# Kernel optimization log

Hardware: AMD Instinct MI355X
Metric: run time of the kernel (lower is better)

## Reference

```python
import jax, jax.numpy as jnp
import numpy as np
import math

D_MODEL = 512
N_HEADS = 8
D_K = D_MODEL // N_HEADS
B, S = 2, 4096
LN_EPS = 1e-5


def _xavier(key, fan_in, fan_out):
    limit = math.sqrt(6.0 / (fan_in + fan_out))
    return jax.random.uniform(key, (fan_in, fan_out), jnp.float32, -limit, limit)


def setup_inputs() -> dict:
    key = jax.random.key(0)
    ks = jax.random.split(key, 12)
    x = jax.random.normal(ks[0], (B, S, D_MODEL), jnp.float32)
    consciousness_state = jax.random.normal(ks[1], (B, D_MODEL), jnp.float32)
    # weights stored as [in, out] (equivalent to torch Linear weight.T)
    w_q = _xavier(ks[2], D_MODEL, D_MODEL)
    w_k = _xavier(ks[3], D_MODEL, D_MODEL)
    w_v = _xavier(ks[4], D_MODEL, D_MODEL)
    w_o = _xavier(ks[5], D_MODEL, D_MODEL)
    b_o = jnp.zeros((D_MODEL,), jnp.float32)
    w_gate = _xavier(ks[6], D_MODEL, N_HEADS)
    b_gate = jnp.zeros((N_HEADS,), jnp.float32)
    w_int = _xavier(ks[7], D_MODEL, D_MODEL)
    b_int = jnp.zeros((D_MODEL,), jnp.float32)
    ln_gamma = jnp.ones((D_MODEL,), jnp.float32)
    ln_beta = jnp.zeros((D_MODEL,), jnp.float32)
    return {"x": x, "consciousness_state": consciousness_state,
            "w_q": w_q, "w_k": w_k, "w_v": w_v, "w_o": w_o, "b_o": b_o,
            "w_gate": w_gate, "b_gate": b_gate, "w_int": w_int, "b_int": b_int,
            "ln_gamma": ln_gamma, "ln_beta": ln_beta}


def reference(x, consciousness_state, w_q, w_k, w_v, w_o, b_o,
              w_gate, b_gate, w_int, b_int, ln_gamma, ln_beta):
    b, s, d = x.shape
    # project and split heads: [B, H, S, d_k]
    def heads(w):
        return (x @ w).reshape(b, s, N_HEADS, D_K).transpose(0, 2, 1, 3)
    Q, K, V = heads(w_q), heads(w_k), heads(w_v)
    scores = jnp.einsum('bhsd,bhtd->bhst', Q, K) / math.sqrt(D_K)  # [B,H,S,S]
    # per-head consciousness gate BEFORE softmax
    cw = jax.nn.sigmoid(consciousness_state @ w_gate + b_gate)  # [B,H]
    scores = scores * cw[:, :, None, None]
    attn = jax.nn.softmax(scores, axis=-1)
    # dropout is identity in eval mode
    context = jnp.einsum('bhst,bhtd->bhsd', attn, V)
    context = context.transpose(0, 2, 1, 3).reshape(b, s, d)
    out = context @ w_o + b_o
    iw = jax.nn.sigmoid(consciousness_state @ w_int + b_int)  # [B,D]
    out = out * iw[:, None, :]
    # residual + LayerNorm
    h = out + x
    mu = jnp.mean(h, axis=-1, keepdims=True)
    var = jnp.var(h, axis=-1, keepdims=True)
    out = (h - mu) * jax.lax.rsqrt(var + LN_EPS) * ln_gamma + ln_beta
    return out, attn.mean(axis=1)
```

## Files before the change

### kernel.cpp

```cpp
#include <hip/hip_runtime.h>
#include <hip/hip_bf16.h>

using short8 = __attribute__((ext_vector_type(8))) short;
using f32x4  = __attribute__((ext_vector_type(4))) float;

#define S_LEN 4096
#define DM 512

__device__ __forceinline__ unsigned short f2b(float f) {
    unsigned int u = __float_as_uint(f);
    u += 0x7fffu + ((u >> 16) & 1u);
    return (unsigned short)(u >> 16);
}

__device__ __forceinline__ short8 pack8(float4 a, float4 b) {
    short8 r;
    r[0] = (short)f2b(a.x); r[1] = (short)f2b(a.y); r[2] = (short)f2b(a.z); r[3] = (short)f2b(a.w);
    r[4] = (short)f2b(b.x); r[5] = (short)f2b(b.y); r[6] = (short)f2b(b.z); r[7] = (short)f2b(b.w);
    return r;
}

__global__ __launch_bounds__(256) void convert_w(
    const float* __restrict__ w0, const float* __restrict__ w1,
    const float* __restrict__ w2, const float* __restrict__ w3,
    unsigned short* __restrict__ t0, unsigned short* __restrict__ t1,
    unsigned short* __restrict__ t2, unsigned short* __restrict__ t3)
{
    __shared__ float sh[64][65];
    const float* src; unsigned short* dst;
    switch (blockIdx.z) {
        case 0: src = w0; dst = t0; break;
        case 1: src = w1; dst = t1; break;
        case 2: src = w2; dst = t2; break;
        default: src = w3; dst = t3; break;
    }
    int k0 = blockIdx.x * 64, n0 = blockIdx.y * 64;
    int tid = threadIdx.x;
    for (int i = tid; i < 4096; i += 256) {
        int k = i >> 6, n = i & 63;
        sh[k][n] = src[(size_t)(k0 + k) * DM + n0 + n];
    }
    __syncthreads();
    for (int i = tid; i < 4096; i += 256) {
        int n = i >> 6, k = i & 63;
        dst[(size_t)(n0 + n) * DM + k0 + k] = f2b(sh[k][n]);
    }
}

__global__ __launch_bounds__(256) void convert_x(
    const float* __restrict__ x, unsigned short* __restrict__ xb)
{
    size_t i = ((size_t)blockIdx.x * 256 + threadIdx.x) * 8;
    float4 a = *reinterpret_cast<const float4*>(x + i);
    float4 b = *reinterpret_cast<const float4*>(x + i + 4);
    *reinterpret_cast<short8*>(xb + i) = pack8(a, b);
}

__global__ __launch_bounds__(64) void gates_kernel(
    const float* __restrict__ cs, const float* __restrict__ wg, const float* __restrict__ bg,
    const float* __restrict__ wi, const float* __restrict__ bi,
    float* __restrict__ cwout, float* __restrict__ iwout)
{
    int o = blockIdx.x, b = blockIdx.y, lane = threadIdx.x;
    const float* c = cs + (size_t)b * DM;
    float acc = 0.f;
    if (o < 8) {
        #pragma unroll
        for (int j = 0; j < 8; ++j) { int k = j * 64 + lane; acc += c[k] * wg[(size_t)k * 8 + o]; }
    } else {
        int n = o - 8;
        #pragma unroll
        for (int j = 0; j < 8; ++j) { int k = j * 64 + lane; acc += c[k] * wi[(size_t)k * DM + n]; }
    }
    #pragma unroll
    for (int d = 32; d; d >>= 1) acc += __shfl_xor(acc, d);
    if (lane == 0) {
        if (o < 8) cwout[b * 8 + o] = 1.f / (1.f + __expf(-(acc + bg[o])));
        else       iwout[b * DM + (o - 8)] = 1.f / (1.f + __expf(-(acc + bi[o - 8])));
    }
}

__global__ __launch_bounds__(256) void gemm_qkv(
    const unsigned short* __restrict__ A, const unsigned short* __restrict__ WT,
    const float* __restrict__ cw,
    unsigned short* __restrict__ Qb, unsigned short* __restrict__ Kb,
    unsigned short* __restrict__ Vt)
{
    __shared__ unsigned short a_sh[64][72];
    __shared__ unsigned short b_sh[64][72];
    const int m0 = blockIdx.x * 64;
    const int n0g = blockIdx.y * 64;
    const int which = blockIdx.y >> 3;
    const int tid = threadIdx.x;
    const int wave = tid >> 6, lane = tid & 63;
    const int g = lane >> 4, lr = lane & 15;
    const int srow = tid >> 3, skc = (tid & 7) * 8;

    float sq = 1.f;
    if (which == 0) {
        int b = blockIdx.x >> 6;
        int h = blockIdx.y & 7;
        sq = cw[b * 8 + h] * 0.125f * 1.44269504f;
    }

    f32x4 acc[4];
    #pragma unroll
    for (int i = 0; i < 4; ++i) acc[i] = (f32x4){0.f, 0.f, 0.f, 0.f};

    short8 ar[2], br[2];
    #pragma unroll
    for (int cc = 0; cc < 2; ++cc) {
        int row = srow + cc * 32;
        ar[cc] = *reinterpret_cast<const short8*>(A  + (size_t)(m0  + row) * DM + skc);
        br[cc] = *reinterpret_cast<const short8*>(WT + (size_t)(n0g + row) * DM + skc);
    }

    for (int k0 = 0; k0 < 512; k0 += 64) {
        #pragma unroll
        for (int cc = 0; cc < 2; ++cc) {
            int row = srow + cc * 32;
            *reinterpret_cast<short8*>(&a_sh[row][skc]) = ar[cc];
            *reinterpret_cast<short8*>(&b_sh[row][skc]) = br[cc];
        }
        __syncthreads();
        if (k0 + 64 < 512) {
            #pragma unroll
            for (int cc = 0; cc < 2; ++cc) {
                int row = srow + cc * 32;
                ar[cc] = *reinterpret_cast<const short8*>(A  + (size_t)(m0  + row) * DM + k0 + 64 + skc);
                br[cc] = *reinterpret_cast<const short8*>(WT + (size_t)(n0g + row) * DM + k0 + 64 + skc);
            }
        }
        __builtin_amdgcn_s_setprio(1);
        #pragma unroll
        for (int ks = 0; ks < 2; ++ks) {
            short8 af = *reinterpret_cast<const short8*>(&a_sh[wave * 16 + lr][ks * 32 + g * 8]);
            #pragma unroll
            for (int nf = 0; nf < 4; ++nf) {
                short8 bf = *reinterpret_cast<const short8*>(&b_sh[nf * 16 + lr][ks * 32 + g * 8]);
                acc[nf] = __builtin_amdgcn_mfma_f32_16x16x32_bf16(af, bf, acc[nf], 0, 0, 0);
            }
        }
        __builtin_amdgcn_s_setprio(0);
        __syncthreads();
    }

    #pragma unroll
    for (int nf = 0; nf < 4; ++nf) {
        #pragma unroll
        for (int r = 0; r < 4; ++r) {
            int m = m0 + wave * 16 + g * 4 + r;
            int nl = (blockIdx.y & 7) * 64 + nf * 16 + lr;
            unsigned short v = f2b(acc[nf][r] * sq);
            if (which == 0) {
                Qb[(size_t)m * DM + nl] = v;
            } else if (which == 1) {
                Kb[(size_t)m * DM + nl] = v;
            } else {
                int b = m >> 12, s = m & 4095;
                int h = nl >> 6, d = nl & 63;
                Vt[((size_t)(b * 8 + h) * 64 + d) * S_LEN + s] = v;
            }
        }
    }
}

__global__ __launch_bounds__(256) void gemm_proj(
    const unsigned short* __restrict__ A, const unsigned short* __restrict__ WT,
    float* __restrict__ outf, const float* __restrict__ bias,
    const float* __restrict__ iw, const float* __restrict__ xres)
{
    __shared__ unsigned short a_sh[64][72];
    __shared__ unsigned short b_sh[64][72];
    const int m0 = blockIdx.x * 64;
    const int n0 = blockIdx.y * 64;
    const int tid = threadIdx.x;
    const int wave = tid >> 6, lane = tid & 63;
    const int g = lane >> 4, lr = lane & 15;
    const int srow = tid >> 3, skc = (tid & 7) * 8;

    f32x4 acc[4];
    #pragma unroll
    for (int i = 0; i < 4; ++i) acc[i] = (f32x4){0.f, 0.f, 0.f, 0.f};

    short8 ar[2], br[2];
    #pragma unroll
    for (int cc = 0; cc < 2; ++cc) {
        int row = srow + cc * 32;
        ar[cc] = *reinterpret_cast<const short8*>(A  + (size_t)(m0 + row) * DM + skc);
        br[cc] = *reinterpret_cast<const short8*>(WT + (size_t)(n0 + row) * DM + skc);
    }

    for (int k0 = 0; k0 < 512; k0 += 64) {
        #pragma unroll
        for (int cc = 0; cc < 2; ++cc) {
            int row = srow + cc * 32;
            *reinterpret_cast<short8*>(&a_sh[row][skc]) = ar[cc];
            *reinterpret_cast<short8*>(&b_sh[row][skc]) = br[cc];
        }
        __syncthreads();
        if (k0 + 64 < 512) {
            #pragma unroll
            for (int cc = 0; cc < 2; ++cc) {
                int row = srow + cc * 32;
                ar[cc] = *reinterpret_cast<const short8*>(A  + (size_t)(m0 + row) * DM + k0 + 64 + skc);
                br[cc] = *reinterpret_cast<const short8*>(WT + (size_t)(n0 + row) * DM + k0 + 64 + skc);
            }
        }
        __builtin_amdgcn_s_setprio(1);
        #pragma unroll
        for (int ks = 0; ks < 2; ++ks) {
            short8 af = *reinterpret_cast<const short8*>(&a_sh[wave * 16 + lr][ks * 32 + g * 8]);
            #pragma unroll
            for (int nf = 0; nf < 4; ++nf) {
                short8 bf = *reinterpret_cast<const short8*>(&b_sh[nf * 16 + lr][ks * 32 + g * 8]);
                acc[nf] = __builtin_amdgcn_mfma_f32_16x16x32_bf16(af, bf, acc[nf], 0, 0, 0);
            }
        }
        __builtin_amdgcn_s_setprio(0);
        __syncthreads();
    }

    #pragma unroll
    for (int nf = 0; nf < 4; ++nf) {
        #pragma unroll
        for (int r = 0; r < 4; ++r) {
            int m = m0 + wave * 16 + g * 4 + r;
            int n = n0 + nf * 16 + lr;
            int b = m >> 12;
            float v = (acc[nf][r] + bias[n]) * iw[b * DM + n] + xres[(size_t)m * DM + n];
            outf[(size_t)m * DM + n] = v;
        }
    }
}

__global__ __launch_bounds__(256) void attn_ctx(
    const unsigned short* __restrict__ Qb, const unsigned short* __restrict__ Kb,
    const unsigned short* __restrict__ Vt,
    float* __restrict__ lbuf, unsigned short* __restrict__ ctx)
{
    __shared__ unsigned short k_sh[64][72];
    __shared__ unsigned short v_sh[64][72];
    __shared__ unsigned short p_sh[4][32][72];
    const int wg = blockIdx.x;
    const int logical = (wg & 7) * 64 + (wg >> 3);
    const int q0 = (logical & 31) * 128;
    const int bh = logical >> 5;
    const int b = bh >> 3, h = bh & 7;
    const int tid = threadIdx.x, wave = tid >> 6, lane = tid & 63;
    const int g = lane >> 4, lr = lane & 15;
    const int srow = tid >> 3, skc = (tid & 7) * 8;

    short8 qf[2][2];
    #pragma unroll
    for (int qq = 0; qq < 2; ++qq) {
        const unsigned short* qp = Qb + (size_t)(b * S_LEN + q0 + wave * 32 + qq * 16 + lr) * DM + h * 64;
        qf[qq][0] = *reinterpret_cast<const short8*>(qp + g * 8);
        qf[qq][1] = *reinterpret_cast<const short8*>(qp + 32 + g * 8);
    }
    short8 onesb;
    #pragma unroll
    for (int i = 0; i < 8; ++i) onesb[i] = (short)0x3F80;

    f32x4 lsum[2];
    f32x4 cacc[2][4];
    #pragma unroll
    for (int qq = 0; qq < 2; ++qq) {
        lsum[qq] = (f32x4){0.f, 0.f, 0.f, 0.f};
        #pragma unroll
        for (int i = 0; i < 4; ++i) cacc[qq][i] = (f32x4){0.f, 0.f, 0.f, 0.f};
    }

    const unsigned short* Kbase = Kb + (size_t)(b * S_LEN) * DM + h * 64;
    const unsigned short* Vbase = Vt + ((size_t)bh * 64) * S_LEN;

    short8 kr[2], vr[2];
    #pragma unroll
    for (int cc = 0; cc < 2; ++cc) {
        int row = srow + cc * 32;
        kr[cc] = *reinterpret_cast<const short8*>(Kbase + (size_t)row * DM + skc);
        vr[cc] = *reinterpret_cast<const short8*>(Vbase + (size_t)row * S_LEN + skc);
    }

    for (int kv0 = 0; kv0 < S_LEN; kv0 += 64) {
        #pragma unroll
        for (int cc = 0; cc < 2; ++cc) {
            int row = srow + cc * 32;
            *reinterpret_cast<short8*>(&k_sh[row][skc]) = kr[cc];
            *reinterpret_cast<short8*>(&v_sh[row][skc]) = vr[cc];
        }
        __syncthreads();
        f32x4 st[2][4];
        #pragma unroll
        for (int qq = 0; qq < 2; ++qq)
            #pragma unroll
            for (int f = 0; f < 4; ++f) st[qq][f] = (f32x4){0.f, 0.f, 0.f, 0.f};
        __builtin_amdgcn_s_setprio(1);
        #pragma unroll
        for (int ks = 0; ks < 2; ++ks) {
            #pragma unroll
            for (int f = 0; f < 4; ++f) {
                short8 kf = *reinterpret_cast<const short8*>(&k_sh[f * 16 + lr][ks * 32 + g * 8]);
                #pragma unroll
                for (int qq = 0; qq < 2; ++qq)
                    st[qq][f] = __builtin_amdgcn_mfma_f32_16x16x32_bf16(kf, qf[qq][ks], st[qq][f], 0, 0, 0);
            }
        }
        __builtin_amdgcn_s_setprio(0);
        if (kv0 + 64 < S_LEN) {
            #pragma unroll
            for (int cc = 0; cc < 2; ++cc) {
                int row = srow + cc * 32;
                kr[cc] = *reinterpret_cast<const short8*>(Kbase + (size_t)(kv0 + 64 + row) * DM + skc);
                vr[cc] = *reinterpret_cast<const short8*>(Vbase + (size_t)row * S_LEN + kv0 + 64 + skc);
            }
        }
        #pragma unroll
        for (int qq = 0; qq < 2; ++qq) {
            #pragma unroll
            for (int f = 0; f < 4; ++f) {
                float p0 = __builtin_amdgcn_exp2f(st[qq][f][0]);
                float p1 = __builtin_amdgcn_exp2f(st[qq][f][1]);
                float p2 = __builtin_amdgcn_exp2f(st[qq][f][2]);
                float p3 = __builtin_amdgcn_exp2f(st[qq][f][3]);
                unsigned u0, u1;
                asm("v_cvt_pk_bf16_f32 %0, %1, %2" : "=v"(u0) : "v"(p0), "v"(p1));
                asm("v_cvt_pk_bf16_f32 %0, %1, %2" : "=v"(u1) : "v"(p2), "v"(p3));
                uint2 pv; pv.x = u0; pv.y = u1;
                *reinterpret_cast<uint2*>(&p_sh[wave][qq * 16 + lr][f * 16 + g * 4]) = pv;
            }
        }
        __builtin_amdgcn_s_setprio(1);
        #pragma unroll
        for (int ks = 0; ks < 2; ++ks) {
            short8 pf[2];
            #pragma unroll
            for (int qq = 0; qq < 2; ++qq)
                pf[qq] = *reinterpret_cast<const short8*>(&p_sh[wave][qq * 16 + lr][ks * 32 + g * 8]);
            #pragma unroll
            for (int qq = 0; qq < 2; ++qq)
                lsum[qq] = __builtin_amdgcn_mfma_f32_16x16x32_bf16(pf[qq], onesb, lsum[qq], 0, 0, 0);
            #pragma unroll
            for (int df = 0; df < 4; ++df) {
                short8 vf = *reinterpret_cast<const short8*>(&v_sh[df * 16 + lr][ks * 32 + g * 8]);
                #pragma unroll
                for (int qq = 0; qq < 2; ++qq)
                    cacc[qq][df] = __builtin_amdgcn_mfma_f32_16x16x32_bf16(pf[qq], vf, cacc[qq][df], 0, 0, 0);
            }
        }
        __builtin_amdgcn_s_setprio(0);
        __syncthreads();
    }
    #pragma unroll
    for (int qq = 0; qq < 2; ++qq) {
        float rl[4];
        #pragma unroll
        for (int r = 0; r < 4; ++r) rl[r] = 1.f / lsum[qq][r];
        if (lr == 0) {
            #pragma unroll
            for (int r = 0; r < 4; ++r)
                lbuf[bh * S_LEN + q0 + wave * 32 + qq * 16 + g * 4 + r] = lsum[qq][r];
        }
        #pragma unroll
        for (int df = 0; df < 4; ++df) {
            #pragma unroll
            for (int r = 0; r < 4; ++r) {
                int q = q0 + wave * 32 + qq * 16 + g * 4 + r;
                ctx[(size_t)(b * S_LEN + q) * DM + h * 64 + df * 16 + lr] = f2b(cacc[qq][df][r] * rl[r]);
            }
        }
    }
}

__global__ __launch_bounds__(256) void attn_mean(
    const unsigned short* __restrict__ Qb, const unsigned short* __restrict__ Kb,
    const float* __restrict__ lbuf, float* __restrict__ outmean)
{
    __shared__ unsigned short k_sh[32][520];
    const int wg = blockIdx.x;
    const int logical = (wg & 7) * 128 + (wg >> 3);
    const int q0 = (logical & 63) * 64;
    const int kcb = logical >> 6;
    const int kc0 = (kcb & 7) * 512;
    const int b = kcb >> 3;
    const int tid = threadIdx.x, wave = tid >> 6, lane = tid & 63;
    const int g = lane >> 4, lr = lane & 15;
    const int srow = tid >> 6, scol = (tid & 63) * 8;

    const int qrow = q0 + wave * 16 + lr;
    float la2[8];
    #pragma unroll
    for (int h = 0; h < 8; ++h)
        la2[h] = -log2f(lbuf[(b * 8 + h) * S_LEN + qrow]) - 3.0f;

    const unsigned short* qbase = Qb + (size_t)(b * S_LEN + qrow) * DM;
    const unsigned short* Kbase = Kb + (size_t)(b * S_LEN) * DM;
    float* obase = outmean + (size_t)(b * S_LEN + qrow) * S_LEN;

    short8 stg[8];
    #pragma unroll
    for (int i = 0; i < 8; ++i) {
        int row = srow + i * 4;
        stg[i] = *reinterpret_cast<const short8*>(Kbase + (size_t)(kc0 + row) * DM + scol);
    }

    for (int t = 0; t < 16; ++t) {
        int kv0 = kc0 + t * 32;
        #pragma unroll
        for (int i = 0; i < 8; ++i) {
            int row = srow + i * 4;
            *reinterpret_cast<short8*>(&k_sh[row][scol]) = stg[i];
        }
        __syncthreads();
        if (t + 1 < 16) {
            #pragma unroll
            for (int i = 0; i < 8; ++i) {
                int row = srow + i * 4;
                stg[i] = *reinterpret_cast<const short8*>(Kbase + (size_t)(kv0 + 32 + row) * DM + scol);
            }
        }
        float macc[2][4];
        #pragma unroll
        for (int f = 0; f < 2; ++f)
            #pragma unroll
            for (int r = 0; r < 4; ++r) macc[f][r] = 0.f;
        #pragma unroll
        for (int h = 0; h < 8; ++h) {
            const unsigned short* qp = qbase + h * 64;
            short8 qf0 = *reinterpret_cast<const short8*>(qp + g * 8);
            short8 qf1 = *reinterpret_cast<const short8*>(qp + 32 + g * 8);
            f32x4 s[2];
            s[0] = (f32x4){0.f, 0.f, 0.f, 0.f};
            s[1] = (f32x4){0.f, 0.f, 0.f, 0.f};
            __builtin_amdgcn_s_setprio(1);
            #pragma unroll
            for (int f = 0; f < 2; ++f) {
                short8 kf0 = *reinterpret_cast<const short8*>(&k_sh[f * 16 + lr][h * 64 + g * 8]);
                s[f] = __builtin_amdgcn_mfma_f32_16x16x32_bf16(kf0, qf0, s[f], 0, 0, 0);
                short8 kf1 = *reinterpret_cast<const short8*>(&k_sh[f * 16 + lr][h * 64 + 32 + g * 8]);
                s[f] = __builtin_amdgcn_mfma_f32_16x16x32_bf16(kf1, qf1, s[f], 0, 0, 0);
            }
            __builtin_amdgcn_s_setprio(0);
            #pragma unroll
            for (int f = 0; f < 2; ++f)
                #pragma unroll
                for (int r = 0; r < 4; ++r)
                    macc[f][r] += __builtin_amdgcn_exp2f(s[f][r] + la2[h]);
        }
        #pragma unroll
        for (int f = 0; f < 2; ++f) {
            float4 ov;
            ov.x = macc[f][0]; ov.y = macc[f][1]; ov.z = macc[f][2]; ov.w = macc[f][3];
            *reinterpret_cast<float4*>(obase + kv0 + f * 16 + g * 4) = ov;
        }
        __syncthreads();
    }
}

__global__ __launch_bounds__(64) void ln_kernel(
    const float* __restrict__ hbuf, const float* __restrict__ gamma,
    const float* __restrict__ beta, float* __restrict__ dout)
{
    int row = blockIdx.x, lane = threadIdx.x;
    const float* hp = hbuf + (size_t)row * DM + lane * 8;
    float4 v0 = *reinterpret_cast<const float4*>(hp);
    float4 v1 = *reinterpret_cast<const float4*>(hp + 4);
    float s = v0.x + v0.y + v0.z + v0.w + v1.x + v1.y + v1.z + v1.w;
    float ss = v0.x * v0.x + v0.y * v0.y + v0.z * v0.z + v0.w * v0.w
             + v1.x * v1.x + v1.y * v1.y + v1.z * v1.z + v1.w * v1.w;
    #pragma unroll
    for (int d = 32; d; d >>= 1) { s += __shfl_xor(s, d); ss += __shfl_xor(ss, d); }
    float mu = s * (1.f / 512.f);
    float var = ss * (1.f / 512.f) - mu * mu;
    float rstd = rsqrtf(var + 1e-5f);
    float4 g0 = *reinterpret_cast<const float4*>(gamma + lane * 8);
    float4 g1 = *reinterpret_cast<const float4*>(gamma + lane * 8 + 4);
    float4 b0 = *reinterpret_cast<const float4*>(beta + lane * 8);
    float4 b1 = *reinterpret_cast<const float4*>(beta + lane * 8 + 4);
    float4 o0, o1;
    o0.x = (v0.x - mu) * rstd * g0.x + b0.x;
    o0.y = (v0.y - mu) * rstd * g0.y + b0.y;
    o0.z = (v0.z - mu) * rstd * g0.z + b0.z;
    o0.w = (v0.w - mu) * rstd * g0.w + b0.w;
    o1.x = (v1.x - mu) * rstd * g1.x + b1.x;
    o1.y = (v1.y - mu) * rstd * g1.y + b1.y;
    o1.z = (v1.z - mu) * rstd * g1.z + b1.z;
    o1.w = (v1.w - mu) * rstd * g1.w + b1.w;
    float* op = dout + (size_t)row * DM + lane * 8;
    *reinterpret_cast<float4*>(op) = o0;
    *reinterpret_cast<float4*>(op + 4) = o1;
}

extern "C" void kernel_launch(void* const* d_in, const int* in_sizes, int n_in,
                              void* d_out, int out_size, void* d_ws, size_t ws_size,
                              hipStream_t stream)
{
    const float* x   = (const float*)d_in[0];
    const float* cs  = (const float*)d_in[1];
    const float* wq  = (const float*)d_in[2];
    const float* wk  = (const float*)d_in[3];
    const float* wv  = (const float*)d_in[4];
    const float* wo  = (const float*)d_in[5];
    const float* bo  = (const float*)d_in[6];
    const float* wg  = (const float*)d_in[7];
    const float* bg  = (const float*)d_in[8];
    const float* wi  = (const float*)d_in[9];
    const float* bi  = (const float*)d_in[10];
    const float* gam = (const float*)d_in[11];
    const float* bet = (const float*)d_in[12];

    float* out = (float*)d_out;
    float* outmean = out + (size_t)2 * S_LEN * DM;

    char* ws = (char*)d_ws;
    size_t off = 0;
    auto alloc = [&](size_t bytes) { void* p = ws + off; off += (bytes + 255) & ~(size_t)255; return p; };

    unsigned short* wtq = (unsigned short*)alloc((size_t)DM * DM * 2);
    unsigned short* wtk = (unsigned short*)alloc((size_t)DM * DM * 2);
    unsigned short* wtv = (unsigned short*)alloc((size_t)DM * DM * 2);
    unsigned short* wto = (unsigned short*)alloc((size_t)DM * DM * 2);
    unsigned short* xb  = (unsigned short*)alloc((size_t)2 * S_LEN * DM * 2);
    unsigned short* Qb  = (unsigned short*)alloc((size_t)2 * S_LEN * DM * 2);
    unsigned short* Kb  = (unsigned short*)alloc((size_t)2 * S_LEN * DM * 2);
    unsigned short* Vt  = (unsigned short*)alloc((size_t)2 * S_LEN * DM * 2);
    unsigned short* ctx = (unsigned short*)alloc((size_t)2 * S_LEN * DM * 2);
    float* lbuf = (float*)alloc((size_t)16 * S_LEN * 4);
    float* cwb  = (float*)alloc(64);
    float* iwb  = (float*)alloc((size_t)2 * DM * 4);
    float* hbuf = (float*)Qb;

    convert_w<<<dim3(8, 8, 4), 256, 0, stream>>>(wq, wk, wv, wo, wtq, wtk, wtv, wto);
    convert_x<<<dim3(2048), 256, 0, stream>>>(x, xb);
    gates_kernel<<<dim3(520, 2), 64, 0, stream>>>(cs, wg, bg, wi, bi, cwb, iwb);

    gemm_qkv<<<dim3(128, 24), 256, 0, stream>>>(xb, wtq, cwb, Qb, Kb, Vt);

    attn_ctx<<<dim3(512), 256, 0, stream>>>(Qb, Kb, Vt, lbuf, ctx);
    attn_mean<<<dim3(1024), 256, 0, stream>>>(Qb, Kb, lbuf, outmean);

    gemm_proj<<<dim3(128, 8), 256, 0, stream>>>(ctx, wto, hbuf, bo, iwb, x);
    ln_kernel<<<dim3(2 * S_LEN), 64, 0, stream>>>(hbuf, gam, bet, out);
}
```

Baseline: 243.6 us.

## Double-buffer K/V shared tiles in attention context kernel to drop a barrier

Turns the K/V shared-memory tiles into two ping-pong buffers. Each iteration now writes the prefetched next tile into the spare buffer after the PV MFMAs, and global loads run two tiles ahead. This removes one __syncthreads per iteration and gives the global loads more time before they are needed. In exchange it doubles K/V LDS use, which may lower occupancy, and keeps the prefetch registers live longer.

Result: no change. 245.4 us (+0.7%).

```diff
diff --git a/kernel.cpp b/kernel.cpp
--- a/kernel.cpp
+++ b/kernel.cpp
@@ -239,8 +239,8 @@
     const unsigned short* __restrict__ Vt,
     float* __restrict__ lbuf, unsigned short* __restrict__ ctx)
 {
-    __shared__ unsigned short k_sh[64][72];
-    __shared__ unsigned short v_sh[64][72];
+    __shared__ unsigned short k_sh[2][64][72];
+    __shared__ unsigned short v_sh[2][64][72];
     __shared__ unsigned short p_sh[4][32][72];
     const int wg = blockIdx.x;
     const int logical = (wg & 7) * 64 + (wg >> 3);
@@ -281,15 +281,22 @@
         kr[cc] = *reinterpret_cast<const short8*>(Kbase + (size_t)row * DM + skc);
         vr[cc] = *reinterpret_cast<const short8*>(Vbase + (size_t)row * S_LEN + skc);
     }
-
-    for (int kv0 = 0; kv0 < S_LEN; kv0 += 64) {
-        #pragma unroll
-        for (int cc = 0; cc < 2; ++cc) {
-            int row = srow + cc * 32;
-            *reinterpret_cast<short8*>(&k_sh[row][skc]) = kr[cc];
-            *reinterpret_cast<short8*>(&v_sh[row][skc]) = vr[cc];
-        }
-        __syncthreads();
+    #pragma unroll
+    for (int cc = 0; cc < 2; ++cc) {
+        int row = srow + cc * 32;
+        *reinterpret_cast<short8*>(&k_sh[0][row][skc]) = kr[cc];
+        *reinterpret_cast<short8*>(&v_sh[0][row][skc]) = vr[cc];
+    }
+    __syncthreads();
+    #pragma unroll
+    for (int cc = 0; cc < 2; ++cc) {
+        int row = srow + cc * 32;
+        kr[cc] = *reinterpret_cast<const short8*>(Kbase + (size_t)(64 + row) * DM + skc);
+        vr[cc] = *reinterpret_cast<const short8*>(Vbase + (size_t)row * S_LEN + 64 + skc);
+    }
+
+    for (int t = 0; t < 64; ++t) {
+        const int cur = t & 1;
         f32x4 st[2][4];
         #pragma unroll
         for (int qq = 0; qq < 2; ++qq)
@@ -300,21 +307,13 @@
         for (int ks = 0; ks < 2; ++ks) {
             #pragma unroll
             for (int f = 0; f < 4; ++f) {
-                short8 kf = *reinterpret_cast<const short8*>(&k_sh[f * 16 + lr][ks * 32 + g * 8]);
+                short8 kf = *reinterpret_cast<const short8*>(&k_sh[cur][f * 16 + lr][ks * 32 + g * 8]);
                 #pragma unroll
                 for (int qq = 0; qq < 2; ++qq)
                     st[qq][f] = __builtin_amdgcn_mfma_f32_16x16x32_bf16(kf, qf[qq][ks], st[qq][f], 0, 0, 0);
             }
         }
         __builtin_amdgcn_s_setprio(0);
-        if (kv0 + 64 < S_LEN) {
-            #pragma unroll
-            for (int cc = 0; cc < 2; ++cc) {
-                int row = srow + cc * 32;
-                kr[cc] = *reinterpret_cast<const short8*>(Kbase + (size_t)(kv0 + 64 + row) * DM + skc);
-                vr[cc] = *reinterpret_cast<const short8*>(Vbase + (size_t)row * S_LEN + kv0 + 64 + skc);
-            }
-        }
         #pragma unroll
         for (int qq = 0; qq < 2; ++qq) {
             #pragma unroll
@@ -342,13 +341,30 @@
                 lsum[qq] = __builtin_amdgcn_mfma_f32_16x16x32_bf16(pf[qq], onesb, lsum[qq], 0, 0, 0);
             #pragma unroll
             for (int df = 0; df < 4; ++df) {
-                short8 vf = *reinterpret_cast<const short8*>(&v_sh[df * 16 + lr][ks * 32 + g * 8]);
+                short8 vf = *reinterpret_cast<const short8*>(&v_sh[cur][df * 16 + lr][ks * 32 + g * 8]);
                 #pragma unroll
                 for (int qq = 0; qq < 2; ++qq)
                     cacc[qq][df] = __builtin_amdgcn_mfma_f32_16x16x32_bf16(pf[qq], vf, cacc[qq][df], 0, 0, 0);
             }
         }
         __builtin_amdgcn_s_setprio(0);
+        if (t + 1 < 64) {
+            #pragma unroll
+            for (int cc = 0; cc < 2; ++cc) {
+                int row = srow + cc * 32;
+                *reinterpret_cast<short8*>(&k_sh[1 - cur][row][skc]) = kr[cc];
+                *reinterpret_cast<short8*>(&v_sh[1 - cur][row][skc]) = vr[cc];
+            }
+            if (t + 2 < 64) {
+                int kvn = (t + 2) * 64;
+                #pragma unroll
+                for (int cc = 0; cc < 2; ++cc) {
+                    int row = srow + cc * 32;
+                    kr[cc] = *reinterpret_cast<const short8*>(Kbase + (size_t)(kvn + row) * DM + skc);
+                    vr[cc] = *reinterpret_cast<const short8*>(Vbase + (size_t)row * S_LEN + kvn + skc);
+                }
+            }
+        }
         __syncthreads();
     }
     #pragma unroll
```

## Load K/V fragments directly from global into registers, dropping LDS staging and barriers

Applied to the files above, without the earlier changes.

The attention-context kernel stops staging K and V tiles through shared memory. Each wave now loads its own MFMA operand fragments straight from global memory into registers and prefetches the next tile during compute, which removes both per-iteration __syncthreads. In exchange, each of the four waves fetches the full K/V tile redundantly (four times the global/L2 traffic), register pressure rises, and the fragment loads are less coalesced than the previous cooperative loads.

New measurement: 378.2 us. 1.55x slower.

```diff
diff --git a/kernel.cpp b/kernel.cpp
--- a/kernel.cpp
+++ b/kernel.cpp
@@ -239,8 +239,6 @@
     const unsigned short* __restrict__ Vt,
     float* __restrict__ lbuf, unsigned short* __restrict__ ctx)
 {
-    __shared__ unsigned short k_sh[64][72];
-    __shared__ unsigned short v_sh[64][72];
     __shared__ unsigned short p_sh[4][32][72];
     const int wg = blockIdx.x;
     const int logical = (wg & 7) * 64 + (wg >> 3);
@@ -249,7 +247,6 @@
     const int b = bh >> 3, h = bh & 7;
     const int tid = threadIdx.x, wave = tid >> 6, lane = tid & 63;
     const int g = lane >> 4, lr = lane & 15;
-    const int srow = tid >> 3, skc = (tid & 7) * 8;
 
     short8 qf[2][2];
     #pragma unroll
@@ -271,25 +268,23 @@
         for (int i = 0; i < 4; ++i) cacc[qq][i] = (f32x4){0.f, 0.f, 0.f, 0.f};
     }
 
-    const unsigned short* Kbase = Kb + (size_t)(b * S_LEN) * DM + h * 64;
-    const unsigned short* Vbase = Vt + ((size_t)bh * 64) * S_LEN;
-
-    short8 kr[2], vr[2];
-    #pragma unroll
-    for (int cc = 0; cc < 2; ++cc) {
-        int row = srow + cc * 32;
-        kr[cc] = *reinterpret_cast<const short8*>(Kbase + (size_t)row * DM + skc);
-        vr[cc] = *reinterpret_cast<const short8*>(Vbase + (size_t)row * S_LEN + skc);
-    }
-
-    for (int kv0 = 0; kv0 < S_LEN; kv0 += 64) {
-        #pragma unroll
-        for (int cc = 0; cc < 2; ++cc) {
-            int row = srow + cc * 32;
-            *reinterpret_cast<short8*>(&k_sh[row][skc]) = kr[cc];
-            *reinterpret_cast<short8*>(&v_sh[row][skc]) = vr[cc];
-        }
-        __syncthreads();
+    const unsigned short* Kl = Kb + (size_t)(b * S_LEN + lr) * DM + h * 64 + g * 8;
+    const unsigned short* Vl = Vt + ((size_t)bh * 64 + lr) * S_LEN + g * 8;
+
+    short8 krf[8], vrf[8];
+    #pragma unroll
+    for (int f = 0; f < 4; ++f)
+        #pragma unroll
+        for (int ks = 0; ks < 2; ++ks)
+            krf[f * 2 + ks] = *reinterpret_cast<const short8*>(Kl + (size_t)(f * 16) * DM + ks * 32);
+    #pragma unroll
+    for (int df = 0; df < 4; ++df)
+        #pragma unroll
+        for (int ks = 0; ks < 2; ++ks)
+            vrf[df * 2 + ks] = *reinterpret_cast<const short8*>(Vl + (size_t)(df * 16) * S_LEN + ks * 32);
+
+    for (int t = 0; t < 64; ++t) {
+        const int kv0 = t * 64;
         f32x4 st[2][4];
         #pragma unroll
         for (int qq = 0; qq < 2; ++qq)
@@ -300,20 +295,18 @@
         for (int ks = 0; ks < 2; ++ks) {
             #pragma unroll
             for (int f = 0; f < 4; ++f) {
-                short8 kf = *reinterpret_cast<const short8*>(&k_sh[f * 16 + lr][ks * 32 + g * 8]);
                 #pragma unroll
                 for (int qq = 0; qq < 2; ++qq)
-                    st[qq][f] = __builtin_amdgcn_mfma_f32_16x16x32_bf16(kf, qf[qq][ks], st[qq][f], 0, 0, 0);
+                    st[qq][f] = __builtin_amdgcn_mfma_f32_16x16x32_bf16(krf[f * 2 + ks], qf[qq][ks], st[qq][f], 0, 0, 0);
             }
         }
         __builtin_amdgcn_s_setprio(0);
-        if (kv0 + 64 < S_LEN) {
-            #pragma unroll
-            for (int cc = 0; cc < 2; ++cc) {
-                int row = srow + cc * 32;
-                kr[cc] = *reinterpret_cast<const short8*>(Kbase + (size_t)(kv0 + 64 + row) * DM + skc);
-                vr[cc] = *reinterpret_cast<const short8*>(Vbase + (size_t)row * S_LEN + kv0 + 64 + skc);
-            }
+        if (t + 1 < 64) {
+            #pragma unroll
+            for (int f = 0; f < 4; ++f)
+                #pragma unroll
+                for (int ks = 0; ks < 2; ++ks)
+                    krf[f * 2 + ks] = *reinterpret_cast<const short8*>(Kl + (size_t)(kv0 + 64 + f * 16) * DM + ks * 32);
         }
         #pragma unroll
         for (int qq = 0; qq < 2; ++qq) {
@@ -342,14 +335,19 @@
                 lsum[qq] = __builtin_amdgcn_mfma_f32_16x16x32_bf16(pf[qq], onesb, lsum[qq], 0, 0, 0);
             #pragma unroll
             for (int df = 0; df < 4; ++df) {
-                short8 vf = *reinterpret_cast<const short8*>(&v_sh[df * 16 + lr][ks * 32 + g * 8]);
                 #pragma unroll
                 for (int qq = 0; qq < 2; ++qq)
-                    cacc[qq][df] = __builtin_amdgcn_mfma_f32_16x16x32_bf16(pf[qq], vf, cacc[qq][df], 0, 0, 0);
+                    cacc[qq][df] = __builtin_amdgcn_mfma_f32_16x16x32_bf16(pf[qq], vrf[df * 2 + ks], cacc[qq][df], 0, 0, 0);
             }
         }
         __builtin_amdgcn_s_setprio(0);
-        __syncthreads();
+        if (t + 1 < 64) {
+            #pragma unroll
+            for (int df = 0; df < 4; ++df)
+                #pragma unroll
+                for (int ks = 0; ks < 2; ++ks)
+                    vrf[df * 2 + ks] = *reinterpret_cast<const short8*>(Vl + (size_t)(df * 16) * S_LEN + kv0 + 64 + ks * 32);
+        }
     }
     #pragma unroll
     for (int qq = 0; qq < 2; ++qq) {
```
